# Optimization experiments

Hardware: AMD Instinct MI355X
Metric: run time of the kernel (lower is better)

## Reference

```python
import jax, jax.numpy as jnp
import numpy as np

HEADS = 16  # matches init_kwargs


def setup_inputs() -> dict:
    key = jax.random.key(0)
    ks = jax.random.split(key, 9)
    N, L, E, D = 2, 2048, 1024, 64
    return {
        "query": jax.random.normal(ks[0], (N, L, E), dtype=jnp.float32),
        "keys": jax.random.normal(ks[1], (N, L, E), dtype=jnp.float32),
        "values": jax.random.normal(ks[2], (N, L, E), dtype=jnp.float32),
        "masks": jax.random.randint(ks[3], (N, 1, 1, L), 0, 2, dtype=jnp.int32),
        "Wq": jax.random.normal(ks[4], (D, D), dtype=jnp.float32) / np.sqrt(D),
        "Wk": jax.random.normal(ks[5], (D, D), dtype=jnp.float32) / np.sqrt(D),
        "Wv": jax.random.normal(ks[6], (D, D), dtype=jnp.float32) / np.sqrt(D),
        "Wo": jax.random.normal(ks[7], (E, E), dtype=jnp.float32) / np.sqrt(E),
        "bo": jax.random.normal(ks[8], (E,), dtype=jnp.float32),
    }


def reference(query, keys, values, masks, Wq, Wk, Wv, Wo, bo):
    N, Lq, E = query.shape
    Lk = keys.shape[1]
    H = HEADS
    D = E // H
    # split heads: [N, L, H, D]
    q = query.reshape(N, Lq, H, D)
    k = keys.reshape(N, Lk, H, D)
    v = values.reshape(N, Lk, H, D)
    # per-head linear projections (weights shared across heads); Linear: x @ W.T
    q = jnp.einsum("nqhd,ed->nqhe", q, Wq)
    k = jnp.einsum("nkhd,ed->nkhe", k, Wk)
    v = jnp.einsum("nkhd,ed->nkhe", v, Wv)
    # scores [N, H, Lq, Lk]
    scores = jnp.einsum("nqhd,nkhd->nhqk", q, k)
    scores = jnp.where(masks == 0, jnp.float32(-1e20), scores)
    # NOTE: original scales by sqrt(embed_size), not sqrt(head_dim)
    attn = jax.nn.softmax(scores / jnp.sqrt(jnp.float32(E)), axis=3)
    out = jnp.einsum("nhqk,nkhd->nqhd", attn, v).reshape(N, Lq, E)
    return out @ Wo.T + bo
```

## Files before the change

### kernel.cpp

```cpp
#include <hip/hip_runtime.h>


typedef __bf16 bf16_t;
typedef __bf16 bf16x4 __attribute__((ext_vector_type(4)));
typedef __bf16 bf16x8 __attribute__((ext_vector_type(8)));
typedef float f32x4 __attribute__((ext_vector_type(4)));
typedef unsigned int u32x4 __attribute__((ext_vector_type(4)));

#define MFMA16(a, b, c) __builtin_amdgcn_mfma_f32_16x16x32_bf16((a), (b), (c), 0, 0, 0)

#define GLOAD_LDS16(gp, lp)                                              \
    __builtin_amdgcn_global_load_lds(                                    \
        (const __attribute__((address_space(1))) void*)(gp),             \
        (__attribute__((address_space(3))) void*)(lp), 16, 0, 0)

__device__ inline bf16x8 cvt8(const float* __restrict__ p) {
    f32x4 a = *(const f32x4*)p;
    f32x4 b = *(const f32x4*)(p + 4);
    bf16x8 r;
    r[0] = (bf16_t)a[0]; r[1] = (bf16_t)a[1];
    r[2] = (bf16_t)a[2]; r[3] = (bf16_t)a[3];
    r[4] = (bf16_t)b[0]; r[5] = (bf16_t)b[1];
    r[6] = (bf16_t)b[2]; r[7] = (bf16_t)b[3];
    return r;
}

__device__ inline bf16x8 cvt8s(const f32x4 a, const f32x4 b) {
    bf16x8 r;
    r[0] = (bf16_t)a[0]; r[1] = (bf16_t)a[1];
    r[2] = (bf16_t)a[2]; r[3] = (bf16_t)a[3];
    r[4] = (bf16_t)b[0]; r[5] = (bf16_t)b[1];
    r[6] = (bf16_t)b[2]; r[7] = (bf16_t)b[3];
    return r;
}

__device__ inline float exp2_fast(float x) {
    float r;
    asm("v_exp_f32 %0, %1" : "=v"(r) : "v"(x));
    return r;
}

__device__ inline unsigned cvt_pk_bf16(float lo, float hi) {
    unsigned r;
    asm("v_cvt_pk_bf16_f32 %0, %1, %2" : "=v"(r) : "v"(lo), "v"(hi));
    return r;
}

__device__ inline void xchg_quads(unsigned &x, unsigned &y) {
    asm("v_permlane32_swap_b32 %0, %1\n\t"
        "v_permlane16_swap_b32 %0, %1"
        : "+v"(x), "+v"(y));
}

__global__ __launch_bounds__(256) void scan_kernel(
    const int* __restrict__ msk, int* __restrict__ excl, int* __restrict__ lmap,
    const float* __restrict__ Wq, const float* __restrict__ Wk,
    const float* __restrict__ Wv,
    bf16_t* __restrict__ Wqb, bf16_t* __restrict__ Wkb, bf16_t* __restrict__ Wvb)
{
    const int t = threadIdx.x;

    if (blockIdx.x >= 2) {
        const int wi = blockIdx.x - 2;
        const float* Ws = (wi == 0) ? Wq : (wi == 1) ? Wk : Wv;
        bf16_t* Wb = (wi == 0) ? Wqb : (wi == 1) ? Wkb : Wvb;
        const float scale = (wi == 0) ? 0.04508422f : 1.0f;
        #pragma unroll
        for (int j = 0; j < 4; j++) {
            int idx = t * 16 + j * 4;
            f32x4 v = *(const f32x4*)&Ws[idx];
            bf16x4 r;
            r[0] = (bf16_t)(v[0] * scale); r[1] = (bf16_t)(v[1] * scale);
            r[2] = (bf16_t)(v[2] * scale); r[3] = (bf16_t)(v[3] * scale);
            *(bf16x4*)&Wb[idx] = r;
        }
        return;
    }

    __shared__ int wsum[4];
    const int n = blockIdx.x;
    const int lane = t & 63, w = t >> 6;
    const int* m = msk + n * 2048;
    int* e = excl + n * 2049;
    int* lm = lmap + n * 2048;

    int v[8], s = 0;
    #pragma unroll
    for (int j = 0; j < 8; j++) { v[j] = (m[t * 8 + j] != 0); s += v[j]; }

    int inc = s;
    #pragma unroll
    for (int d = 1; d < 64; d <<= 1) {
        int o = __shfl_up(inc, d);
        if (lane >= d) inc += o;
    }
    if (lane == 63) wsum[w] = inc;
    __syncthreads();
    int off = 0;
    #pragma unroll
    for (int i = 0; i < 4; i++)
        if (i < w) off += wsum[i];

    int a = off + inc - s;
    #pragma unroll
    for (int j = 0; j < 8; j++) {
        e[t * 8 + j] = a;
        if (v[j]) lm[a] = t * 8 + j;
        a += v[j];
    }
    if (t == 255) e[2048] = a;
}

__global__ __launch_bounds__(256) void qkv_proj_kernel(
    const float* __restrict__ qin, const float* __restrict__ kin,
    const float* __restrict__ vin,
    const bf16_t* __restrict__ Wqb, const bf16_t* __restrict__ Wkb,
    const bf16_t* __restrict__ Wvb, const float* __restrict__ Wo,
    const int* __restrict__ excl, const int* __restrict__ lmap,
    bf16_t* __restrict__ qp, bf16_t* __restrict__ kc, bf16_t* __restrict__ vcT,
    bf16_t* __restrict__ Wob)
{
    __shared__ __align__(16) char smem[51200];

    const int t = threadIdx.x;
    const int w = t >> 6, lane = t & 63, quad = lane >> 4, l16 = lane & 15;

    if (blockIdx.y == 3) {
        int idx = blockIdx.x * 1024 + t * 4;
        f32x4 v = *(const f32x4*)&Wo[idx];
        bf16x4 r;
        r[0] = (bf16_t)v[0]; r[1] = (bf16_t)v[1];
        r[2] = (bf16_t)v[2]; r[3] = (bf16_t)v[3];
        *(bf16x4*)&Wob[idx] = r;
        return;
    }

    if (blockIdx.y == 2) {
        bf16_t* Ct = (bf16_t*)smem;
        const int h = blockIdx.x & 15;
        const int ctile = blockIdx.x >> 4;
        const int n = ctile >> 5;
        const int c0 = (ctile & 31) * 64;
        const int Lc = excl[n * 2049 + 2048];
        if (c0 >= Lc) return;

        const int p0 = w * 16 + l16;
        int cs = c0 + p0; if (cs > Lc - 1) cs = Lc - 1;
        const int tg = lmap[n * 2048 + cs];
        const size_t rb = ((size_t)(n * 2048 + tg)) * 1024 + h * 64;

        bf16x8 b0 = cvt8(&vin[rb + quad * 8]);
        bf16x8 b1 = cvt8(&vin[rb + 32 + quad * 8]);

        #pragma unroll
        for (int nt = 0; nt < 4; nt++) {
            bf16x8 a0 = *(const bf16x8*)&Wvb[(nt * 16 + l16) * 64 + quad * 8];
            bf16x8 a1 = *(const bf16x8*)&Wvb[(nt * 16 + l16) * 64 + 32 + quad * 8];
            f32x4 acc = {0.f, 0.f, 0.f, 0.f};
            acc = MFMA16(a0, b0, acc);
            acc = MFMA16(a1, b1, acc);
            #pragma unroll
            for (int r = 0; r < 4; r++)
                Ct[(nt * 16 + quad * 4 + r) * 72 + w * 16 + l16] = (bf16_t)acc[r];
        }
        __syncthreads();
        const int p = t & 63, rg = t >> 6;
        const int cnt = (Lc - c0 < 64) ? (Lc - c0) : 64;
        if (p < cnt) {
            size_t ob = ((size_t)(n * 16 + h)) * 131072 + c0 + p;
            #pragma unroll
            for (int rr = 0; rr < 16; rr++) {
                int r = rg * 16 + rr;
                vcT[ob + (size_t)r * 2048] = Ct[r * 72 + p];
            }
        }
        return;
    }

    if (blockIdx.x >= 512) return;
    const bool isK = (blockIdx.y == 1);
    const float* x; const bf16_t* Wb;
    int n = 0, c0 = 0, Lc = 0;
    if (!isK) { x = qin; Wb = Wqb; }
    else {
        x = kin; Wb = Wkb;
        n = blockIdx.x >> 8;
        c0 = (blockIdx.x & 255) * 8;
        Lc = excl[n * 2049 + 2048];
        if (c0 >= Lc) return;
    }

    float* Xs = (float*)smem;
    bf16_t* Ct2 = (bf16_t*)(smem + 32768);

    const int g0 = blockIdx.x * 128;

    #pragma unroll
    for (int j = 0; j < 8; j++) {
        int br = w * 32 + j * 4;
        int srow = br + (lane >> 4);
        int scol = ((lane & 15) ^ (srow & 15)) * 4;
        size_t gaddr;
        if (!isK) {
            gaddr = (size_t)(g0 + srow) * 64 + scol;
        } else {
            int csx = c0 + (srow >> 4); if (csx > Lc - 1) csx = Lc - 1;
            int hs = srow & 15;
            int ls = lmap[n * 2048 + csx];
            gaddr = ((size_t)((n * 2048 + ls) * 16 + hs)) * 64 + scol;
        }
        GLOAD_LDS16(&x[gaddr], &Xs[br * 64]);
    }
    __syncthreads();

    const int rbase = w * 32;
    bf16x8 a[2][2];
    #pragma unroll
    for (int qs = 0; qs < 2; qs++) {
        int row = rbase + qs * 16 + l16;
        const char* rowp = (const char*)Xs + (size_t)row * 256;
        int swb = (row & 15) << 4;
        #pragma unroll
        for (int c = 0; c < 2; c++) {
            f32x4 lo = *(const f32x4*)(rowp + ((c * 128 + quad * 32) ^ swb));
            f32x4 hi = *(const f32x4*)(rowp + ((c * 128 + quad * 32 + 16) ^ swb));
            a[qs][c] = cvt8s(lo, hi);
        }
    }

    f32x4 acc[4][2];
    #pragma unroll
    for (int nt = 0; nt < 4; nt++) {
        bf16x8 b0 = *(const bf16x8*)&Wb[(nt * 16 + l16) * 64 + quad * 8];
        bf16x8 b1 = *(const bf16x8*)&Wb[(nt * 16 + l16) * 64 + 32 + quad * 8];
        #pragma unroll
        for (int qs = 0; qs < 2; qs++) {
            f32x4 z = {0.f, 0.f, 0.f, 0.f};
            z = MFMA16(a[qs][0], b0, z);
            z = MFMA16(a[qs][1], b1, z);
            acc[nt][qs] = z;
        }
    }

    #pragma unroll
    for (int nt = 0; nt < 4; nt++)
        #pragma unroll
        for (int qs = 0; qs < 2; qs++)
            #pragma unroll
            for (int r = 0; r < 4; r++)
                Ct2[(rbase + qs * 16 + quad * 4 + r) * 72 + nt * 16 + l16] = (bf16_t)acc[nt][qs][r];
    __syncthreads();

    #pragma unroll
    for (int it = 0; it < 4; it++) {
        int j = it * 32 + (t >> 3);
        bf16x8 val = *(const bf16x8*)&Ct2[j * 72 + (t & 7) * 8];
        if (isK) {
            int c = c0 + (j >> 4), h2 = j & 15;
            if (c < Lc)
                *(bf16x8*)&kc[(((size_t)(n * 16 + h2)) * 2048 + c) * 64 + (t & 7) * 8] = val;
        } else {
            int g = g0 + j, h2 = g & 15, token = g >> 4;
            int n2 = token >> 11, l = token & 2047;
            *(bf16x8*)&qp[(((size_t)(n2 * 16 + h2)) * 2048 + l) * 64 + (t & 7) * 8] = val;
        }
    }
}

__global__ __launch_bounds__(256) void attn_kernel(
    const bf16_t* __restrict__ qp, const bf16_t* __restrict__ kc,
    const bf16_t* __restrict__ vcT, const int* __restrict__ excl,
    bf16_t* __restrict__ ao)
{
    __shared__ bf16_t Kt[2][128][64];
    __shared__ bf16_t Vt[2][64][128];

    const int t = threadIdx.x;
    const int w = t >> 6, lane = t & 63, quad = lane >> 4, l16 = lane & 15;

    const int flat = blockIdx.x;
    const int xcd = flat & 7, slot = flat >> 3;
    const int nh = xcd * 4 + (slot >> 4), qb = slot & 15;
    const int n = nh >> 4, h = nh & 15;
    const int qbase = qb * 128 + w * 32;
    const size_t nhbase = (size_t)nh * 131072;

    const int Lc = excl[n * 2049 + 2048];
    const int ntiles = (Lc + 127) >> 7;

    const int ksrow = lane >> 3;
    const int kscol = ((lane & 7) ^ (lane >> 3)) * 8;
    const int swr = l16 & 7;
    const int ck0 = (quad ^ swr) * 8;
    const int ck1 = ((quad + 4) ^ swr) * 8;

    bf16x8 aq[2][2];
    #pragma unroll
    for (int qs = 0; qs < 2; qs++)
        #pragma unroll
        for (int c = 0; c < 2; c++)
            aq[qs][c] = *(const bf16x8*)&qp[nhbase + (size_t)(qbase + qs * 16 + l16) * 64 + c * 32 + quad * 8];

    f32x4 o[2][4];
    float lsum[2] = {0.f, 0.f};
    #pragma unroll
    for (int qs = 0; qs < 2; qs++)
        #pragma unroll
        for (int dt = 0; dt < 4; dt++) {
            o[qs][dt][0] = 0.f; o[qs][dt][1] = 0.f; o[qs][dt][2] = 0.f; o[qs][dt][3] = 0.f;
        }

#define STAGE_KV(buf, kn)                                                     \
    {                                                                         \
        _Pragma("unroll")                                                     \
        for (int j = 0; j < 4; j++) {                                         \
            int rb = w * 32 + j * 8;                                          \
            GLOAD_LDS16(&kc[nhbase + (size_t)((kn) + rb + ksrow) * 64 + kscol],\
                        &Kt[buf][rb][0]);                                     \
        }                                                                     \
        _Pragma("unroll")                                                     \
        for (int j = 0; j < 4; j++) {                                         \
            int rb = w * 16 + j * 4;                                          \
            int d = rb + (lane >> 4);                                         \
            int sc = ((lane & 15) ^ (d & 15)) * 8;                            \
            GLOAD_LDS16(&vcT[nhbase + (size_t)d * 2048 + (kn) + sc],          \
                        &Vt[buf][rb][0]);                                     \
        }                                                                     \
    }

    STAGE_KV(0, 0);

    for (int i = 0; i < ntiles; i++) {
        const int cb = i & 1, nb = cb ^ 1;
        const int k0 = i * 128;
        __syncthreads();

        if (i + 1 < ntiles) STAGE_KV(nb, k0 + 128);

        #pragma unroll
        for (int hf = 0; hf < 2; hf++) {
            const int kh = k0 + hf * 64;

            f32x4 st[2][4];
            __builtin_amdgcn_s_setprio(1);
            #pragma unroll
            for (int ct = 0; ct < 4; ct++) {
                bf16x8 kb0 = *(const bf16x8*)&Kt[cb][hf * 64 + ct * 16 + l16][ck0];
                bf16x8 kb1 = *(const bf16x8*)&Kt[cb][hf * 64 + ct * 16 + l16][ck1];
                #pragma unroll
                for (int qs = 0; qs < 2; qs++) {
                    f32x4 acc = {0.f, 0.f, 0.f, 0.f};
                    acc = MFMA16(kb0, aq[qs][0], acc);
                    acc = MFMA16(kb1, aq[qs][1], acc);
                    st[qs][ct] = acc;
                }
            }
            __builtin_amdgcn_s_setprio(0);

            if (kh + 64 <= Lc) {
                #pragma unroll
                for (int qs = 0; qs < 2; qs++)
                    #pragma unroll
                    for (int ct = 0; ct < 4; ct++)
                        #pragma unroll
                        for (int r = 0; r < 4; r++) {
                            float p = exp2_fast(st[qs][ct][r]);
                            lsum[qs] += p;
                            st[qs][ct][r] = p;
                        }
            } else {
                #pragma unroll
                for (int qs = 0; qs < 2; qs++)
                    #pragma unroll
                    for (int ct = 0; ct < 4; ct++)
                        #pragma unroll
                        for (int r = 0; r < 4; r++) {
                            int kk = kh + ct * 16 + quad * 4 + r;
                            float p = (kk < Lc) ? exp2_fast(st[qs][ct][r]) : 0.0f;
                            lsum[qs] += p;
                            st[qs][ct][r] = p;
                        }
            }

            bf16x8 bp[2][2];
            #pragma unroll
            for (int qs = 0; qs < 2; qs++) {
                unsigned u[4][2];
                #pragma unroll
                for (int ct = 0; ct < 4; ct++) {
                    u[ct][0] = cvt_pk_bf16(st[qs][ct][0], st[qs][ct][1]);
                    u[ct][1] = cvt_pk_bf16(st[qs][ct][2], st[qs][ct][3]);
                }
                #pragma unroll
                for (int hh = 0; hh < 2; hh++) {
                    unsigned b0 = u[2 * hh][0], b2 = u[2 * hh + 1][0];
                    xchg_quads(b0, b2);
                    unsigned b1 = u[2 * hh][1], b3 = u[2 * hh + 1][1];
                    xchg_quads(b1, b3);
                    u32x4 q4 = {b0, b1, b2, b3};
                    bp[qs][hh] = __builtin_bit_cast(bf16x8, q4);
                }
            }

            __builtin_amdgcn_s_setprio(1);
            #pragma unroll
            for (int dt = 0; dt < 4; dt++) {
                bf16x8 va0 = *(const bf16x8*)&Vt[cb][dt * 16 + l16][((hf * 8 + quad) ^ l16) * 8];
                bf16x8 va1 = *(const bf16x8*)&Vt[cb][dt * 16 + l16][((hf * 8 + 4 + quad) ^ l16) * 8];
                #pragma unroll
                for (int qs = 0; qs < 2; qs++) {
                    o[qs][dt] = MFMA16(va0, bp[qs][0], o[qs][dt]);
                    o[qs][dt] = MFMA16(va1, bp[qs][1], o[qs][dt]);
                }
            }
            __builtin_amdgcn_s_setprio(0);
        }
    }

    #pragma unroll
    for (int qs = 0; qs < 2; qs++) {
        float v = lsum[qs];
        v += __shfl_xor(v, 16);
        v += __shfl_xor(v, 32);
        float inv = 1.0f / v;
        const int q = qbase + qs * 16 + l16;
        const size_t base = ((size_t)n * 2048 + q) * 1024 + h * 64;
        #pragma unroll
        for (int dt = 0; dt < 4; dt++) {
            bf16x4 ov;
            #pragma unroll
            for (int r = 0; r < 4; r++) ov[r] = (bf16_t)(o[qs][dt][r] * inv);
            *(bf16x4*)&ao[base + dt * 16 + quad * 4] = ov;
        }
    }
}

__global__ __launch_bounds__(256, 2) void out_proj_kernel(
    const bf16_t* __restrict__ X, const bf16_t* __restrict__ Wob,
    const float* __restrict__ bo, float* __restrict__ out)
{
    __shared__ bf16_t Xs[2][128][64];
    __shared__ bf16_t Ws[2][128][64];

    const int t = threadIdx.x;
    const int w = t >> 6, lane = t & 63, quad = lane >> 4, l16 = lane & 15;
    const int Mbase = blockIdx.x * 128;
    const int Nbase = blockIdx.y * 128;
    const int mrow = (w & 1) * 64;
    const int ncol = (w >> 1) * 64;

    const int scol = ((lane & 7) ^ (lane >> 3)) * 8;
    const int swr  = l16 & 7;

    f32x4 acc[4][4];
    #pragma unroll
    for (int mi = 0; mi < 4; mi++)
        #pragma unroll
        for (int ni = 0; ni < 4; ni++) {
            acc[mi][ni][0] = 0.f; acc[mi][ni][1] = 0.f;
            acc[mi][ni][2] = 0.f; acc[mi][ni][3] = 0.f;
        }

    #pragma unroll
    for (int j = 0; j < 4; j++) {
        int br = w * 32 + j * 8;
        GLOAD_LDS16(&X[(size_t)(Mbase + br + (lane >> 3)) * 1024 + scol], &Xs[0][br][0]);
        GLOAD_LDS16(&Wob[(size_t)(Nbase + br + (lane >> 3)) * 1024 + scol], &Ws[0][br][0]);
    }

    for (int i = 0; i < 16; i++) {
        const int cb = i & 1, nb = cb ^ 1;
        __syncthreads();

        if (i < 15) {
            const int kn = (i + 1) * 64;
            #pragma unroll
            for (int j = 0; j < 4; j++) {
                int br = w * 32 + j * 8;
                GLOAD_LDS16(&X[(size_t)(Mbase + br + (lane >> 3)) * 1024 + kn + scol],
                            &Xs[nb][br][0]);
                GLOAD_LDS16(&Wob[(size_t)(Nbase + br + (lane >> 3)) * 1024 + kn + scol],
                            &Ws[nb][br][0]);
            }
        }

        #pragma unroll
        for (int c = 0; c < 2; c++) {
            bf16x8 bfr[4];
            #pragma unroll
            for (int ni = 0; ni < 4; ni++)
                bfr[ni] = *(const bf16x8*)&Ws[cb][ncol + ni * 16 + l16][((c * 4 + quad) ^ swr) * 8];
            #pragma unroll
            for (int mi = 0; mi < 4; mi++) {
                bf16x8 afr = *(const bf16x8*)&Xs[cb][mrow + mi * 16 + l16][((c * 4 + quad) ^ swr) * 8];
                #pragma unroll
                for (int ni = 0; ni < 4; ni++)
                    acc[mi][ni] = MFMA16(afr, bfr[ni], acc[mi][ni]);
            }
        }
    }

    #pragma unroll
    for (int ni = 0; ni < 4; ni++) {
        float b = bo[Nbase + ncol + ni * 16 + l16];
        #pragma unroll
        for (int mi = 0; mi < 4; mi++) {
            #pragma unroll
            for (int r = 0; r < 4; r++) {
                int row = Mbase + mrow + mi * 16 + quad * 4 + r;
                out[(size_t)row * 1024 + Nbase + ncol + ni * 16 + l16] = acc[mi][ni][r] + b;
            }
        }
    }
}

extern "C" void kernel_launch(void* const* d_in, const int* in_sizes, int n_in,
                              void* d_out, int out_size, void* d_ws, size_t ws_size,
                              hipStream_t stream)
{
    const float* qin = (const float*)d_in[0];
    const float* kin = (const float*)d_in[1];
    const float* vin = (const float*)d_in[2];
    const int*   msk = (const int*)d_in[3];
    const float* Wq  = (const float*)d_in[4];
    const float* Wk  = (const float*)d_in[5];
    const float* Wv  = (const float*)d_in[6];
    const float* Wo  = (const float*)d_in[7];
    const float* bo  = (const float*)d_in[8];
    float* out = (float*)d_out;

    bf16_t* ws  = (bf16_t*)d_ws;
    bf16_t* qp  = ws;
    bf16_t* kc  = ws + 4194304;
    bf16_t* vcT = ws + 8388608;
    bf16_t* ao  = ws + 12582912;
    bf16_t* Wob = ws + 16777216;
    int* excl   = (int*)(ws + 17825792);
    int* lmap   = excl + 4100;
    bf16_t* Wqb = (bf16_t*)(lmap + 4096);
    bf16_t* Wkb = Wqb + 4096;
    bf16_t* Wvb = Wkb + 4096;

    scan_kernel<<<5, 256, 0, stream>>>(msk, excl, lmap, Wq, Wk, Wv, Wqb, Wkb, Wvb);
    qkv_proj_kernel<<<dim3(1024, 4), 256, 0, stream>>>(qin, kin, vin, Wqb, Wkb, Wvb, Wo,
                                                        excl, lmap, qp, kc, vcT, Wob);
    attn_kernel<<<dim3(512), 256, 0, stream>>>(qp, kc, vcT, excl, ao);
    out_proj_kernel<<<dim3(32, 8), 256, 0, stream>>>(ao, Wob, bo, out);
}
```

Measured before the change: 165.7 us.

## Fuse Q projection into attention kernel and vectorize V-transpose stores

Measured after the change: 158.4 us. 4.4% less time.

```diff
diff --git a/kernel.cpp b/kernel.cpp
--- a/kernel.cpp
+++ b/kernel.cpp
@@ -112,20 +112,18 @@
 }
 
 __global__ __launch_bounds__(256) void qkv_proj_kernel(
-    const float* __restrict__ qin, const float* __restrict__ kin,
-    const float* __restrict__ vin,
-    const bf16_t* __restrict__ Wqb, const bf16_t* __restrict__ Wkb,
-    const bf16_t* __restrict__ Wvb, const float* __restrict__ Wo,
+    const float* __restrict__ kin, const float* __restrict__ vin,
+    const bf16_t* __restrict__ Wkb, const bf16_t* __restrict__ Wvb,
+    const float* __restrict__ Wo,
     const int* __restrict__ excl, const int* __restrict__ lmap,
-    bf16_t* __restrict__ qp, bf16_t* __restrict__ kc, bf16_t* __restrict__ vcT,
-    bf16_t* __restrict__ Wob)
+    bf16_t* __restrict__ kc, bf16_t* __restrict__ vcT, bf16_t* __restrict__ Wob)
 {
     __shared__ __align__(16) char smem[51200];
 
     const int t = threadIdx.x;
     const int w = t >> 6, lane = t & 63, quad = lane >> 4, l16 = lane & 15;
 
-    if (blockIdx.y == 3) {
+    if (blockIdx.y == 2) {
         int idx = blockIdx.x * 1024 + t * 4;
         f32x4 v = *(const f32x4*)&Wo[idx];
         bf16x4 r;
@@ -135,7 +133,7 @@
         return;
     }
 
-    if (blockIdx.y == 2) {
+    if (blockIdx.y == 1) {
         bf16_t* Ct = (bf16_t*)smem;
         const int h = blockIdx.x & 15;
         const int ctile = blockIdx.x >> 4;
@@ -164,52 +162,43 @@
                 Ct[(nt * 16 + quad * 4 + r) * 72 + w * 16 + l16] = (bf16_t)acc[r];
         }
         __syncthreads();
-        const int p = t & 63, rg = t >> 6;
         const int cnt = (Lc - c0 < 64) ? (Lc - c0) : 64;
-        if (p < cnt) {
-            size_t ob = ((size_t)(n * 16 + h)) * 131072 + c0 + p;
-            #pragma unroll
-            for (int rr = 0; rr < 16; rr++) {
-                int r = rg * 16 + rr;
-                vcT[ob + (size_t)r * 2048] = Ct[r * 72 + p];
+        const size_t ob2 = ((size_t)(n * 16 + h)) * 131072 + c0;
+        #pragma unroll
+        for (int pass = 0; pass < 2; pass++) {
+            int r = pass * 32 + (t >> 3);
+            int cb8 = (t & 7) * 8;
+            if (cb8 < cnt) {
+                if (cb8 + 8 <= cnt) {
+                    *(bf16x8*)&vcT[ob2 + (size_t)r * 2048 + cb8] =
+                        *(const bf16x8*)&Ct[r * 72 + cb8];
+                } else {
+                    for (int q = cb8; q < cnt; q++)
+                        vcT[ob2 + (size_t)r * 2048 + q] = Ct[r * 72 + q];
+                }
             }
         }
         return;
     }
 
     if (blockIdx.x >= 512) return;
-    const bool isK = (blockIdx.y == 1);
-    const float* x; const bf16_t* Wb;
-    int n = 0, c0 = 0, Lc = 0;
-    if (!isK) { x = qin; Wb = Wqb; }
-    else {
-        x = kin; Wb = Wkb;
-        n = blockIdx.x >> 8;
-        c0 = (blockIdx.x & 255) * 8;
-        Lc = excl[n * 2049 + 2048];
-        if (c0 >= Lc) return;
-    }
+    const int n = blockIdx.x >> 8;
+    const int c0 = (blockIdx.x & 255) * 8;
+    const int Lc = excl[n * 2049 + 2048];
+    if (c0 >= Lc) return;
 
     float* Xs = (float*)smem;
     bf16_t* Ct2 = (bf16_t*)(smem + 32768);
-
-    const int g0 = blockIdx.x * 128;
 
     #pragma unroll
     for (int j = 0; j < 8; j++) {
         int br = w * 32 + j * 4;
         int srow = br + (lane >> 4);
         int scol = ((lane & 15) ^ (srow & 15)) * 4;
-        size_t gaddr;
-        if (!isK) {
-            gaddr = (size_t)(g0 + srow) * 64 + scol;
-        } else {
-            int csx = c0 + (srow >> 4); if (csx > Lc - 1) csx = Lc - 1;
-            int hs = srow & 15;
-            int ls = lmap[n * 2048 + csx];
-            gaddr = ((size_t)((n * 2048 + ls) * 16 + hs)) * 64 + scol;
-        }
-        GLOAD_LDS16(&x[gaddr], &Xs[br * 64]);
+        int csx = c0 + (srow >> 4); if (csx > Lc - 1) csx = Lc - 1;
+        int hs = srow & 15;
+        int ls = lmap[n * 2048 + csx];
+        GLOAD_LDS16(&kin[((size_t)((n * 2048 + ls) * 16 + hs)) * 64 + scol], &Xs[br * 64]);
     }
     __syncthreads();
 
@@ -231,8 +220,8 @@
     f32x4 acc[4][2];
     #pragma unroll
     for (int nt = 0; nt < 4; nt++) {
-        bf16x8 b0 = *(const bf16x8*)&Wb[(nt * 16 + l16) * 64 + quad * 8];
-        bf16x8 b1 = *(const bf16x8*)&Wb[(nt * 16 + l16) * 64 + 32 + quad * 8];
+        bf16x8 b0 = *(const bf16x8*)&Wkb[(nt * 16 + l16) * 64 + quad * 8];
+        bf16x8 b1 = *(const bf16x8*)&Wkb[(nt * 16 + l16) * 64 + 32 + quad * 8];
         #pragma unroll
         for (int qs = 0; qs < 2; qs++) {
             f32x4 z = {0.f, 0.f, 0.f, 0.f};
@@ -255,25 +244,22 @@
     for (int it = 0; it < 4; it++) {
         int j = it * 32 + (t >> 3);
         bf16x8 val = *(const bf16x8*)&Ct2[j * 72 + (t & 7) * 8];
-        if (isK) {
-            int c = c0 + (j >> 4), h2 = j & 15;
-            if (c < Lc)
-                *(bf16x8*)&kc[(((size_t)(n * 16 + h2)) * 2048 + c) * 64 + (t & 7) * 8] = val;
-        } else {
-            int g = g0 + j, h2 = g & 15, token = g >> 4;
-            int n2 = token >> 11, l = token & 2047;
-            *(bf16x8*)&qp[(((size_t)(n2 * 16 + h2)) * 2048 + l) * 64 + (t & 7) * 8] = val;
-        }
+        int c = c0 + (j >> 4), h2 = j & 15;
+        if (c < Lc)
+            *(bf16x8*)&kc[(((size_t)(n * 16 + h2)) * 2048 + c) * 64 + (t & 7) * 8] = val;
     }
 }
 
 __global__ __launch_bounds__(256) void attn_kernel(
-    const bf16_t* __restrict__ qp, const bf16_t* __restrict__ kc,
-    const bf16_t* __restrict__ vcT, const int* __restrict__ excl,
-    bf16_t* __restrict__ ao)
+    const float* __restrict__ qin, const bf16_t* __restrict__ Wqb,
+    const bf16_t* __restrict__ kc, const bf16_t* __restrict__ vcT,
+    const int* __restrict__ excl, bf16_t* __restrict__ ao)
 {
-    __shared__ bf16_t Kt[2][128][64];
-    __shared__ bf16_t Vt[2][64][128];
+    __shared__ __align__(16) char smem[65536];
+    bf16_t* KtP = (bf16_t*)smem;
+    bf16_t* VtP = (bf16_t*)(smem + 32768);
+#define KT(buf, r, c) KtP[(buf) * 8192 + (r) * 64 + (c)]
+#define VT(buf, r, c) VtP[(buf) * 8192 + (r) * 128 + (c)]
 
     const int t = threadIdx.x;
     const int w = t >> 6, lane = t & 63, quad = lane >> 4, l16 = lane & 15;
@@ -287,28 +273,85 @@
 
     const int Lc = excl[n * 2049 + 2048];
     const int ntiles = (Lc + 127) >> 7;
+    const int rbase = w * 32;
+
+    bf16x8 aq[2][2];
+    {
+        float* Xq = (float*)smem;
+        bf16_t* Qt = (bf16_t*)(smem + 32768);
+        const int qrow0 = qb * 128;
+        #pragma unroll
+        for (int j = 0; j < 8; j++) {
+            int br = w * 32 + j * 4;
+            int srow = br + (lane >> 4);
+            int scol = ((lane & 15) ^ (srow & 15)) * 4;
+            GLOAD_LDS16(&qin[((size_t)(n * 2048 + qrow0 + srow)) * 1024 + h * 64 + scol],
+                        &Xq[br * 64]);
+        }
+        __syncthreads();
+
+        bf16x8 a[2][2];
+        #pragma unroll
+        for (int qs = 0; qs < 2; qs++) {
+            int row = rbase + qs * 16 + l16;
+            const char* rowp = (const char*)Xq + (size_t)row * 256;
+            int swb = (row & 15) << 4;
+            #pragma unroll
+            for (int c = 0; c < 2; c++) {
+                f32x4 lo = *(const f32x4*)(rowp + ((c * 128 + quad * 32) ^ swb));
+                f32x4 hi = *(const f32x4*)(rowp + ((c * 128 + quad * 32 + 16) ^ swb));
+                a[qs][c] = cvt8s(lo, hi);
+            }
+        }
+        f32x4 pacc[4][2];
+        #pragma unroll
+        for (int nt = 0; nt < 4; nt++) {
+            bf16x8 b0 = *(const bf16x8*)&Wqb[(nt * 16 + l16) * 64 + quad * 8];
+            bf16x8 b1 = *(const bf16x8*)&Wqb[(nt * 16 + l16) * 64 + 32 + quad * 8];
+            #pragma unroll
+            for (int qs = 0; qs < 2; qs++) {
+                f32x4 z = {0.f, 0.f, 0.f, 0.f};
+                z = MFMA16(a[qs][0], b0, z);
+                z = MFMA16(a[qs][1], b1, z);
+                pacc[nt][qs] = z;
+            }
+        }
+        #pragma unroll
+        for (int nt = 0; nt < 4; nt++)
+            #pragma unroll
+            for (int qs = 0; qs < 2; qs++)
+                #pragma unroll
+                for (int r = 0; r < 4; r++) {
+                    int row = rbase + qs * 16 + quad * 4 + r;
+                    int col = nt * 16 + l16;
+                    int byteoff = row * 128 + ((((col >> 3) ^ (row & 7)) << 4) | ((col & 7) << 1));
+                    *(bf16_t*)((char*)Qt + byteoff) = (bf16_t)pacc[nt][qs][r];
+                }
+        #pragma unroll
+        for (int qs = 0; qs < 2; qs++) {
+            int row = rbase + qs * 16 + l16;
+            #pragma unroll
+            for (int c = 0; c < 2; c++)
+                aq[qs][c] = *(const bf16x8*)((const char*)Qt + row * 128 +
+                                             (((c * 4 + quad) ^ (row & 7)) << 4));
+        }
+        __syncthreads();
+    }
+
+    f32x4 o[2][4];
+    float lsum[2] = {0.f, 0.f};
+    #pragma unroll
+    for (int qs = 0; qs < 2; qs++)
+        #pragma unroll
+        for (int dt = 0; dt < 4; dt++) {
+            o[qs][dt][0] = 0.f; o[qs][dt][1] = 0.f; o[qs][dt][2] = 0.f; o[qs][dt][3] = 0.f;
+        }
 
     const int ksrow = lane >> 3;
     const int kscol = ((lane & 7) ^ (lane >> 3)) * 8;
     const int swr = l16 & 7;
     const int ck0 = (quad ^ swr) * 8;
     const int ck1 = ((quad + 4) ^ swr) * 8;
-
-    bf16x8 aq[2][2];
-    #pragma unroll
-    for (int qs = 0; qs < 2; qs++)
-        #pragma unroll
-        for (int c = 0; c < 2; c++)
-            aq[qs][c] = *(const bf16x8*)&qp[nhbase + (size_t)(qbase + qs * 16 + l16) * 64 + c * 32 + quad * 8];
-
-    f32x4 o[2][4];
-    float lsum[2] = {0.f, 0.f};
-    #pragma unroll
-    for (int qs = 0; qs < 2; qs++)
-        #pragma unroll
-        for (int dt = 0; dt < 4; dt++) {
-            o[qs][dt][0] = 0.f; o[qs][dt][1] = 0.f; o[qs][dt][2] = 0.f; o[qs][dt][3] = 0.f;
-        }
 
 #define STAGE_KV(buf, kn)                                                     \
     {                                                                         \
@@ -316,7 +359,7 @@
         for (int j = 0; j < 4; j++) {                                         \
             int rb = w * 32 + j * 8;                                          \
             GLOAD_LDS16(&kc[nhbase + (size_t)((kn) + rb + ksrow) * 64 + kscol],\
-                        &Kt[buf][rb][0]);                                     \
+                        &KT(buf, rb, 0));                                     \
         }                                                                     \
         _Pragma("unroll")                                                     \
         for (int j = 0; j < 4; j++) {                                         \
@@ -324,7 +367,7 @@
             int d = rb + (lane >> 4);                                         \
             int sc = ((lane & 15) ^ (d & 15)) * 8;                            \
             GLOAD_LDS16(&vcT[nhbase + (size_t)d * 2048 + (kn) + sc],          \
-                        &Vt[buf][rb][0]);                                     \
+                        &VT(buf, rb, 0));                                     \
         }                                                                     \
     }
 
@@ -345,8 +388,8 @@
             __builtin_amdgcn_s_setprio(1);
             #pragma unroll
             for (int ct = 0; ct < 4; ct++) {
-                bf16x8 kb0 = *(const bf16x8*)&Kt[cb][hf * 64 + ct * 16 + l16][ck0];
-                bf16x8 kb1 = *(const bf16x8*)&Kt[cb][hf * 64 + ct * 16 + l16][ck1];
+                bf16x8 kb0 = *(const bf16x8*)&KT(cb, hf * 64 + ct * 16 + l16, ck0);
+                bf16x8 kb1 = *(const bf16x8*)&KT(cb, hf * 64 + ct * 16 + l16, ck1);
                 #pragma unroll
                 for (int qs = 0; qs < 2; qs++) {
                     f32x4 acc = {0.f, 0.f, 0.f, 0.f};
@@ -405,8 +448,8 @@
             __builtin_amdgcn_s_setprio(1);
             #pragma unroll
             for (int dt = 0; dt < 4; dt++) {
-                bf16x8 va0 = *(const bf16x8*)&Vt[cb][dt * 16 + l16][((hf * 8 + quad) ^ l16) * 8];
-                bf16x8 va1 = *(const bf16x8*)&Vt[cb][dt * 16 + l16][((hf * 8 + 4 + quad) ^ l16) * 8];
+                bf16x8 va0 = *(const bf16x8*)&VT(cb, dt * 16 + l16, ((hf * 8 + quad) ^ l16) * 8);
+                bf16x8 va1 = *(const bf16x8*)&VT(cb, dt * 16 + l16, ((hf * 8 + 4 + quad) ^ l16) * 8);
                 #pragma unroll
                 for (int qs = 0; qs < 2; qs++) {
                     o[qs][dt] = MFMA16(va0, bp[qs][0], o[qs][dt]);
@@ -423,7 +466,7 @@
         v += __shfl_xor(v, 16);
         v += __shfl_xor(v, 32);
         float inv = 1.0f / v;
-        const int q = qbase + qs * 16 + l16;
+        const int q = qb * 128 + w * 32 + qs * 16 + l16;
         const size_t base = ((size_t)n * 2048 + q) * 1024 + h * 64;
         #pragma unroll
         for (int dt = 0; dt < 4; dt++) {
@@ -433,6 +476,9 @@
             *(bf16x4*)&ao[base + dt * 16 + quad * 4] = ov;
         }
     }
+#undef KT
+#undef VT
+#undef STAGE_KV
 }
 
 __global__ __launch_bounds__(256, 2) void out_proj_kernel(
@@ -530,7 +576,6 @@
     float* out = (float*)d_out;
 
     bf16_t* ws  = (bf16_t*)d_ws;
-    bf16_t* qp  = ws;
     bf16_t* kc  = ws + 4194304;
     bf16_t* vcT = ws + 8388608;
     bf16_t* ao  = ws + 12582912;
@@ -542,8 +587,8 @@
     bf16_t* Wvb = Wkb + 4096;
 
     scan_kernel<<<5, 256, 0, stream>>>(msk, excl, lmap, Wq, Wk, Wv, Wqb, Wkb, Wvb);
-    qkv_proj_kernel<<<dim3(1024, 4), 256, 0, stream>>>(qin, kin, vin, Wqb, Wkb, Wvb, Wo,
-                                                        excl, lmap, qp, kc, vcT, Wob);
-    attn_kernel<<<dim3(512), 256, 0, stream>>>(qp, kc, vcT, excl, ao);
+    qkv_proj_kernel<<<dim3(1024, 3), 256, 0, stream>>>(kin, vin, Wkb, Wvb, Wo,
+                                                        excl, lmap, kc, vcT, Wob);
+    attn_kernel<<<dim3(512), 256, 0, stream>>>(qin, Wqb, kc, vcT, excl, ao);
     out_proj_kernel<<<dim3(32, 8), 256, 0, stream>>>(ao, Wob, bo, out);
 }
```
